# Kernel optimization log

Hardware: AMD Instinct MI355X
Metric: run time of the kernel (lower is better)

The kernel has to match this reference:

```python
import jax, jax.numpy as jnp
import numpy as np

N_NODES = 100000
N_EDGES = 1000000
DIM = 128
N_RELS = 500
N_TIMES = 1000


def setup_inputs() -> dict:
    key = jax.random.key(0)
    ks = jax.random.split(key, 8)
    h = jax.random.normal(ks[0], (N_NODES, DIM), dtype=jnp.float32)
    edge_index = jax.random.randint(ks[1], (2, N_EDGES), 0, N_NODES, dtype=jnp.int64)
    edge_type = jax.random.randint(ks[2], (N_EDGES,), 0, N_RELS, dtype=jnp.int64)
    edge_time = jax.random.randint(ks[3], (N_EDGES,), 0, N_TIMES, dtype=jnp.int64)
    query_rel = 7
    rel_table = jax.random.normal(ks[4], (N_RELS, DIM), dtype=jnp.float32)
    time_table = jax.random.normal(ks[5], (N_TIMES, DIM), dtype=jnp.float32)
    # Linear weights stored as [in, out] so y = x @ W + b
    W1 = jax.random.normal(ks[6], (4 * DIM, DIM), dtype=jnp.float32) * (1.0 / np.sqrt(4 * DIM))
    b1 = jnp.zeros((DIM,), dtype=jnp.float32)
    W2 = jax.random.normal(ks[7], (DIM, 1), dtype=jnp.float32) * (1.0 / np.sqrt(DIM))
    b2 = jnp.zeros((1,), dtype=jnp.float32)
    return {"h": h, "edge_index": edge_index, "edge_type": edge_type,
            "edge_time": edge_time, "query_rel": query_rel,
            "rel_table": rel_table, "time_table": time_table,
            "W1": W1, "b1": b1, "W2": W2, "b2": b2}


def reference(h, edge_index, edge_type, edge_time, query_rel,
              rel_table, time_table, W1, b1, W2, b2):
    src = edge_index[0]                    # [E]
    h_s = h[src]                           # [E, D] gather
    h_r = rel_table[edge_type]             # [E, D] embedding lookup
    h_t = time_table[edge_time]            # [E, D] embedding lookup
    h_rq = jnp.broadcast_to(rel_table[query_rel][None, :], h_s.shape)  # [E, D]
    x = jnp.concatenate([h_s, h_r, h_rq, h_t], axis=1)  # [E, 4D]
    hidden = jax.nn.relu(x @ W1 + b1)      # [E, D]
    alpha = hidden @ W2 + b2               # [E, 1]
    return jax.nn.sigmoid(alpha)[:, 0]     # [E]
```

## Files before the change

kernel.cpp:

```cpp
#include <hip/hip_runtime.h>
#include <hip/hip_fp16.h>
#include <hip/hip_fp8.h>
#include <math.h>

#define DIM 128

typedef _Float16 half8 __attribute__((ext_vector_type(8)));
typedef _Float16 half2v __attribute__((ext_vector_type(2)));
typedef float floatx4 __attribute__((ext_vector_type(4)));


__global__ __launch_bounds__(256) void precompute(
    const float* __restrict__ h, const float* __restrict__ rel,
    const float* __restrict__ tim, const int* __restrict__ qrel,
    const float* __restrict__ W1, const float* __restrict__ b1,
    unsigned char* __restrict__ H8, __half* __restrict__ Rh, __half* __restrict__ Th,
    int n_nodes, int n_rels, int n_times, int nHB, int nRB)
{
    const int tid = threadIdx.x;
    const int b = blockIdx.x;

    const float* A; int M, k0, row0; bool isR = false, isH = false;
    __half* Out = nullptr;
    if (b < nHB)            { A = h;   isH = true; M = n_nodes; k0 = 0;   row0 = b * 128; }
    else if (b < nHB + nRB) { A = rel; Out = Rh;   M = n_rels;  k0 = 128; row0 = (b - nHB) * 128; isR = true; }
    else                    { A = tim; Out = Th;   M = n_times; k0 = 384; row0 = (b - nHB - nRB) * 128; }

    __shared__ _Float16 fragB[32 * 64 * 8];
    __shared__ float c0f[DIM];

#pragma unroll
    for (int it = 0; it < 8; ++it) {
        const int o = tid + it * 256;
        const int ctkc = o >> 6, L = o & 63;
        const int ct = ctkc >> 2, kc = ctkc & 3;
        const int q = L >> 4, n15 = L & 15;
        const float* base = W1 + (size_t)(k0 + kc * 32 + q * 8) * DIM + ct * 16 + n15;
        half8 f;
#pragma unroll
        for (int j = 0; j < 8; ++j) f[j] = (_Float16)base[(size_t)j * DIM];
        *(half8*)&fragB[o * 8] = f;
    }
    if (isR && tid < DIM) {
        const int q = qrel[0];
        const float* hq = rel + (size_t)q * DIM;
        float s = b1[tid];
        for (int k = 0; k < DIM; ++k)
            s = fmaf(hq[k], W1[(size_t)(256 + k) * DIM + tid], s);
        c0f[tid] = s;
    }
    __syncthreads();

    const int w = tid >> 6;
    const int lane = tid & 63;
    const int m15 = lane & 15, q = lane >> 4;

    const float* aBase[2];
#pragma unroll
    for (int mt = 0; mt < 2; ++mt) {
        int arow = row0 + w * 32 + mt * 16 + m15;
        if (arow >= M) arow = M - 1;
        aBase[mt] = A + (size_t)arow * DIM + q * 8;
    }

    floatx4 acc[2][8];
#pragma unroll
    for (int mt = 0; mt < 2; ++mt)
#pragma unroll
        for (int ct = 0; ct < 8; ++ct) acc[mt][ct] = (floatx4)0.f;

#pragma unroll
    for (int kc = 0; kc < 4; ++kc) {
        half8 af[2];
#pragma unroll
        for (int mt = 0; mt < 2; ++mt) {
            const float4 a0 = *(const float4*)(aBase[mt] + kc * 32);
            const float4 a1 = *(const float4*)(aBase[mt] + kc * 32 + 4);
            af[mt][0] = (_Float16)a0.x; af[mt][1] = (_Float16)a0.y;
            af[mt][2] = (_Float16)a0.z; af[mt][3] = (_Float16)a0.w;
            af[mt][4] = (_Float16)a1.x; af[mt][5] = (_Float16)a1.y;
            af[mt][6] = (_Float16)a1.z; af[mt][7] = (_Float16)a1.w;
        }
#pragma unroll
        for (int ct = 0; ct < 8; ++ct) {
            const half8 bf = *(half8*)&fragB[(((ct * 4 + kc) * 64) + lane) * 8];
            acc[0][ct] = __builtin_amdgcn_mfma_f32_16x16x32_f16(af[0], bf, acc[0][ct], 0, 0, 0);
            acc[1][ct] = __builtin_amdgcn_mfma_f32_16x16x32_f16(af[1], bf, acc[1][ct], 0, 0, 0);
        }
    }

    float cadd[8];
#pragma unroll
    for (int ct = 0; ct < 8; ++ct) cadd[ct] = isR ? c0f[ct * 16 + m15] : 0.f;

#pragma unroll
    for (int mt = 0; mt < 2; ++mt)
#pragma unroll
        for (int r = 0; r < 4; ++r) {
            const int m = row0 + w * 32 + mt * 16 + q * 4 + r;
            if (m < M) {
                if (isH) {
                    uint2 pk;
#if __has_builtin(__builtin_amdgcn_cvt_pk_fp8_f32)
                    int w0 = 0, w1 = 0;
                    w0 = __builtin_amdgcn_cvt_pk_fp8_f32(acc[mt][0][r], acc[mt][1][r], w0, false);
                    w0 = __builtin_amdgcn_cvt_pk_fp8_f32(acc[mt][2][r], acc[mt][3][r], w0, true);
                    w1 = __builtin_amdgcn_cvt_pk_fp8_f32(acc[mt][4][r], acc[mt][5][r], w1, false);
                    w1 = __builtin_amdgcn_cvt_pk_fp8_f32(acc[mt][6][r], acc[mt][7][r], w1, true);
                    pk.x = (unsigned)w0; pk.y = (unsigned)w1;
#else
                    union { uint2 u; unsigned char bb[8]; } pu;
#pragma unroll
                    for (int ct = 0; ct < 8; ++ct)
                        pu.bb[ct] = __hip_fp8_e4m3(acc[mt][ct][r]).__x;
                    pk = pu.u;
#endif
                    *(uint2*)(H8 + (size_t)m * DIM + m15 * 8) = pk;
                } else {
                    half8 hv;
#pragma unroll
                    for (int ct = 0; ct < 8; ++ct)
                        hv[ct] = (_Float16)(acc[mt][ct][r] + cadd[ct]);
                    *(half8*)(Out + (size_t)m * DIM + m15 * 8) = hv;
                }
            }
        }
}

__device__ __forceinline__ half2v fp8x2_to_h2(unsigned u16) {
#if __has_builtin(__builtin_amdgcn_cvt_pk_f16_fp8)
    auto c = __builtin_amdgcn_cvt_pk_f16_fp8((short)u16);
    half2v r; r[0] = c[0]; r[1] = c[1];
    return r;
#else
    auto f = __builtin_amdgcn_cvt_pk_f32_fp8((int)u16, false);
    half2v r; r[0] = (_Float16)f[0]; r[1] = (_Float16)f[1];
    return r;
#endif
}

__device__ __forceinline__ float edot(uint2 hu, uint4 ru, uint4 tu,
                                      const half2v* __restrict__ w2h) {
    union U { uint4 u; half2v h[4]; };
    U R, T; R.u = ru; T.u = tu;
    const half2v z = (half2v)(_Float16)0.f;
    const unsigned hw[4] = {hu.x & 0xffffu, hu.x >> 16, hu.y & 0xffffu, hu.y >> 16};
    float p = 0.f;
#pragma unroll
    for (int j = 0; j < 4; ++j) {
        const half2v hh = fp8x2_to_h2(hw[j]);
        half2v s = hh + R.h[j] + T.h[j];
        s = __builtin_elementwise_max(s, z);
#if __has_builtin(__builtin_amdgcn_fdot2)
        p = __builtin_amdgcn_fdot2(s, w2h[j], p, false);
#else
        p = fmaf((float)s[0], (float)w2h[j][0], p);
        p = fmaf((float)s[1], (float)w2h[j][1], p);
#endif
    }
    return p;
}

template<int CTRL>
__device__ __forceinline__ float dpp_row_add(float x) {
    int s = __builtin_amdgcn_update_dpp(0, __float_as_int(x), CTRL, 0xf, 0xf, true);
    return x + __int_as_float(s);
}

__global__ __launch_bounds__(256) void edge_kernel(
    const int* __restrict__ ei, const int* __restrict__ ety,
    const int* __restrict__ eti,
    const unsigned char* __restrict__ H8, const __half* __restrict__ Rh,
    const __half* __restrict__ Th,
    const float* __restrict__ W2, const float* __restrict__ b2,
    float* __restrict__ out, int E, int nGrpTotal)
{
    const int tid = threadIdx.x;
    const int l = tid & 15;
    int g = blockIdx.x * 16 + (tid >> 4);
    const int nQuad = (E + 3) >> 2;
    if (g >= nQuad) return;

    half2v w2h[4];
#pragma unroll
    for (int j = 0; j < 4; ++j) {
        w2h[j][0] = (_Float16)W2[(2 * j) * 16 + l];
        w2h[j][1] = (_Float16)W2[(2 * j + 1) * 16 + l];
    }
    const float b2v = b2[0];
    const bool exact = (E & 3) == 0;
    const unsigned char* Rh8 = (const unsigned char*)Rh;
    const unsigned char* Th8 = (const unsigned char*)Th;

    int s[4], r[4], t[4];
    {
        const int e0 = 4 * g;
        if (exact || e0 + 3 < E) {
#pragma unroll
            for (int i = 0; i < 4; ++i) { s[i] = ei[e0 + i]; r[i] = ety[e0 + i]; t[i] = eti[e0 + i]; }
        } else {
#pragma unroll
            for (int i = 0; i < 4; ++i) {
                const int e = min(e0 + i, E - 1);
                s[i] = ei[e]; r[i] = ety[e]; t[i] = eti[e];
            }
        }
    }

    while (true) {
        const int gn = g + nGrpTotal;
        uint2 hv[4]; uint4 rv[4], tv[4];
#pragma unroll
        for (int i = 0; i < 4; ++i) {
            hv[i] = *(const uint2*)(H8  + ((unsigned)s[i] << 7) + (l << 3));
            rv[i] = *(const uint4*)(Rh8 + ((unsigned)r[i] << 8) + (l << 4));
            tv[i] = *(const uint4*)(Th8 + ((unsigned)t[i] << 8) + (l << 4));
        }
        if (gn < nQuad) {
            const int e0 = 4 * gn;
            if (exact || e0 + 3 < E) {
#pragma unroll
                for (int i = 0; i < 4; ++i) { s[i] = ei[e0 + i]; r[i] = ety[e0 + i]; t[i] = eti[e0 + i]; }
            } else {
#pragma unroll
                for (int i = 0; i < 4; ++i) {
                    const int e = min(e0 + i, E - 1);
                    s[i] = ei[e]; r[i] = ety[e]; t[i] = eti[e];
                }
            }
        }
        float p[4];
#pragma unroll
        for (int i = 0; i < 4; ++i)
            p[i] = edot(hv[i], rv[i], tv[i], w2h);
#pragma unroll
        for (int i = 0; i < 4; ++i) {
            p[i] = dpp_row_add<0x111>(p[i]);
            p[i] = dpp_row_add<0x112>(p[i]);
            p[i] = dpp_row_add<0x114>(p[i]);
            p[i] = dpp_row_add<0x118>(p[i]);
        }
        if (l == 15) {
            const int e0 = 4 * g;
            float4 o;
            o.x = 1.f / (1.f + __expf(-(p[0] + b2v)));
            o.y = 1.f / (1.f + __expf(-(p[1] + b2v)));
            o.z = 1.f / (1.f + __expf(-(p[2] + b2v)));
            o.w = 1.f / (1.f + __expf(-(p[3] + b2v)));
            if (e0 + 3 < E) {
                *(float4*)(out + e0) = o;
            } else {
                const float ov[4] = {o.x, o.y, o.z, o.w};
                for (int i = 0; i < 4 && e0 + i < E; ++i) out[e0 + i] = ov[i];
            }
        }
        if (gn >= nQuad) break;
        g = gn;
    }
}

extern "C" void kernel_launch(void* const* d_in, const int* in_sizes, int n_in,
                              void* d_out, int out_size, void* d_ws, size_t ws_size,
                              hipStream_t stream) {
    const float* h          = (const float*)d_in[0];
    const int*   edge_index = (const int*)d_in[1];
    const int*   edge_type  = (const int*)d_in[2];
    const int*   edge_time  = (const int*)d_in[3];
    const int*   query_rel  = (const int*)d_in[4];
    const float* rel_table  = (const float*)d_in[5];
    const float* time_table = (const float*)d_in[6];
    const float* W1         = (const float*)d_in[7];
    const float* b1         = (const float*)d_in[8];
    const float* W2         = (const float*)d_in[9];
    const float* b2         = (const float*)d_in[10];
    float* out = (float*)d_out;

    const int n_nodes = in_sizes[0] / DIM;
    const int E       = in_sizes[2];
    const int n_rels  = in_sizes[5] / DIM;
    const int n_times = in_sizes[6] / DIM;

    unsigned char* H8 = (unsigned char*)d_ws;
    __half* Rh = (__half*)(H8 + (((size_t)n_nodes * DIM + 255) & ~(size_t)255));
    __half* Th = Rh + (size_t)n_rels * DIM;

    const int nHB = (n_nodes + 127) / 128;
    const int nRB = (n_rels + 127) / 128;
    const int nTB = (n_times + 127) / 128;

    precompute<<<nHB + nRB + nTB, 256, 0, stream>>>(
        h, rel_table, time_table, query_rel, W1, b1,
        H8, Rh, Th, n_nodes, n_rels, n_times, nHB, nRB);

    const int nBlk = 4096;
    edge_kernel<<<nBlk, 256, 0, stream>>>(
        edge_index, edge_type, edge_time, H8, Rh, Th, W2, b2,
        out, E, nBlk * 16);
}
```

Baseline: 160.0 us.

## Cache relation table in LDS and use persistent 1024-thread blocks

The edge kernel now stages the fp16 relation table (500 rows) in shared memory, so relation gathers read LDS instead of global memory. The launch changes to 256 persistent blocks of 1024 threads. Index loads become vectorized nontemporal loads and the output store becomes nontemporal. In exchange each block pays a 128KB LDS fill, and the large LDS footprint limits occupancy to one block per CU.

```diff
diff --git a/kernel.cpp b/kernel.cpp
--- a/kernel.cpp
+++ b/kernel.cpp
@@ -4,10 +4,12 @@
 #include <math.h>
 
 #define DIM 128
+#define LDS_RELS 500
 
 typedef _Float16 half8 __attribute__((ext_vector_type(8)));
 typedef _Float16 half2v __attribute__((ext_vector_type(2)));
 typedef float floatx4 __attribute__((ext_vector_type(4)));
+typedef int intx4 __attribute__((ext_vector_type(4)));
 
 
 __global__ __launch_bounds__(256) void precompute(
@@ -167,95 +169,109 @@
     return x + __int_as_float(s);
 }
 
-__global__ __launch_bounds__(256) void edge_kernel(
+__device__ __forceinline__ void load_idx4(
+    const int* __restrict__ ei, const int* __restrict__ ety,
+    const int* __restrict__ eti, int g, int E, bool exact,
+    int (&s)[4], int (&r)[4], int (&t)[4])
+{
+    const int e0 = 4 * g;
+    if (exact || e0 + 3 < E) {
+        const intx4 a = __builtin_nontemporal_load((const intx4*)(ei + e0));
+        const intx4 b = __builtin_nontemporal_load((const intx4*)(ety + e0));
+        const intx4 c = __builtin_nontemporal_load((const intx4*)(eti + e0));
+#pragma unroll
+        for (int i = 0; i < 4; ++i) { s[i] = a[i]; r[i] = b[i]; t[i] = c[i]; }
+    } else {
+#pragma unroll
+        for (int i = 0; i < 4; ++i) {
+            const int e = min(e0 + i, E - 1);
+            s[i] = ei[e]; r[i] = ety[e]; t[i] = eti[e];
+        }
+    }
+}
+
+__global__ __launch_bounds__(1024) void edge_kernel(
     const int* __restrict__ ei, const int* __restrict__ ety,
     const int* __restrict__ eti,
     const unsigned char* __restrict__ H8, const __half* __restrict__ Rh,
     const __half* __restrict__ Th,
     const float* __restrict__ W2, const float* __restrict__ b2,
-    float* __restrict__ out, int E, int nGrpTotal)
+    float* __restrict__ out, int E, int n_rels, int nGrpTotal)
 {
+    __shared__ uint4 ldsR[LDS_RELS * 16];
+
     const int tid = threadIdx.x;
+
+    {
+        const uint4* Rg = (const uint4*)Rh;
+        const int n4 = min(n_rels, LDS_RELS) * 16;
+        for (int i = tid; i < n4; i += 1024) ldsR[i] = Rg[i];
+    }
+    __syncthreads();
+
     const int l = tid & 15;
-    int g = blockIdx.x * 16 + (tid >> 4);
+    int g = blockIdx.x * 64 + (tid >> 4);
     const int nQuad = (E + 3) >> 2;
-    if (g >= nQuad) return;
-
-    half2v w2h[4];
-#pragma unroll
-    for (int j = 0; j < 4; ++j) {
-        w2h[j][0] = (_Float16)W2[(2 * j) * 16 + l];
-        w2h[j][1] = (_Float16)W2[(2 * j + 1) * 16 + l];
-    }
-    const float b2v = b2[0];
-    const bool exact = (E & 3) == 0;
-    const unsigned char* Rh8 = (const unsigned char*)Rh;
-    const unsigned char* Th8 = (const unsigned char*)Th;
-
-    int s[4], r[4], t[4];
-    {
-        const int e0 = 4 * g;
-        if (exact || e0 + 3 < E) {
-#pragma unroll
-            for (int i = 0; i < 4; ++i) { s[i] = ei[e0 + i]; r[i] = ety[e0 + i]; t[i] = eti[e0 + i]; }
-        } else {
+    if (g < nQuad) {
+        half2v w2h[4];
+#pragma unroll
+        for (int j = 0; j < 4; ++j) {
+            w2h[j][0] = (_Float16)W2[(2 * j) * 16 + l];
+            w2h[j][1] = (_Float16)W2[(2 * j + 1) * 16 + l];
+        }
+        const float b2v = b2[0];
+        const bool exact = (E & 3) == 0;
+        const unsigned char* Th8 = (const unsigned char*)Th;
+        const unsigned char* Rh8 = (const unsigned char*)Rh;
+
+        int s[4], r[4], t[4];
+        load_idx4(ei, ety, eti, g, E, exact, s, r, t);
+
+        while (true) {
+            const int gn = g + nGrpTotal;
+            uint2 hv[4]; uint4 tv[4];
 #pragma unroll
             for (int i = 0; i < 4; ++i) {
-                const int e = min(e0 + i, E - 1);
-                s[i] = ei[e]; r[i] = ety[e]; t[i] = eti[e];
-            }
-        }
-    }
-
-    while (true) {
-        const int gn = g + nGrpTotal;
-        uint2 hv[4]; uint4 rv[4], tv[4];
-#pragma unroll
-        for (int i = 0; i < 4; ++i) {
-            hv[i] = *(const uint2*)(H8  + ((unsigned)s[i] << 7) + (l << 3));
-            rv[i] = *(const uint4*)(Rh8 + ((unsigned)r[i] << 8) + (l << 4));
-            tv[i] = *(const uint4*)(Th8 + ((unsigned)t[i] << 8) + (l << 4));
-        }
-        if (gn < nQuad) {
-            const int e0 = 4 * gn;
-            if (exact || e0 + 3 < E) {
-#pragma unroll
-                for (int i = 0; i < 4; ++i) { s[i] = ei[e0 + i]; r[i] = ety[e0 + i]; t[i] = eti[e0 + i]; }
-            } else {
-#pragma unroll
-                for (int i = 0; i < 4; ++i) {
-                    const int e = min(e0 + i, E - 1);
-                    s[i] = ei[e]; r[i] = ety[e]; t[i] = eti[e];
+                hv[i] = *(const uint2*)(H8  + ((unsigned)s[i] << 7) + (l << 3));
+                tv[i] = *(const uint4*)(Th8 + ((unsigned)t[i] << 8) + (l << 4));
+            }
+            uint4 rv[4];
+#pragma unroll
+            for (int i = 0; i < 4; ++i) {
+                if (r[i] < LDS_RELS) rv[i] = ldsR[(unsigned)r[i] * 16 + l];
+                else rv[i] = *(const uint4*)(Rh8 + ((unsigned)r[i] << 8) + (l << 4));
+            }
+            if (gn < nQuad)
+                load_idx4(ei, ety, eti, gn, E, exact, s, r, t);
+
+            float p[4];
+#pragma unroll
+            for (int i = 0; i < 4; ++i)
+                p[i] = edot(hv[i], rv[i], tv[i], w2h);
+#pragma unroll
+            for (int i = 0; i < 4; ++i) {
+                p[i] = dpp_row_add<0x111>(p[i]);
+                p[i] = dpp_row_add<0x112>(p[i]);
+                p[i] = dpp_row_add<0x114>(p[i]);
+                p[i] = dpp_row_add<0x118>(p[i]);
+            }
+            if (l == 15) {
+                const int e0 = 4 * g;
+                floatx4 o;
+                o[0] = 1.f / (1.f + __expf(-(p[0] + b2v)));
+                o[1] = 1.f / (1.f + __expf(-(p[1] + b2v)));
+                o[2] = 1.f / (1.f + __expf(-(p[2] + b2v)));
+                o[3] = 1.f / (1.f + __expf(-(p[3] + b2v)));
+                if (e0 + 3 < E) {
+                    __builtin_nontemporal_store(o, (floatx4*)(out + e0));
+                } else {
+                    const float ov[4] = {o[0], o[1], o[2], o[3]};
+                    for (int i = 0; i < 4 && e0 + i < E; ++i) out[e0 + i] = ov[i];
                 }
             }
-        }
-        float p[4];
-#pragma unroll
-        for (int i = 0; i < 4; ++i)
-            p[i] = edot(hv[i], rv[i], tv[i], w2h);
-#pragma unroll
-        for (int i = 0; i < 4; ++i) {
-            p[i] = dpp_row_add<0x111>(p[i]);
-            p[i] = dpp_row_add<0x112>(p[i]);
-            p[i] = dpp_row_add<0x114>(p[i]);
-            p[i] = dpp_row_add<0x118>(p[i]);
-        }
-        if (l == 15) {
-            const int e0 = 4 * g;
-            float4 o;
-            o.x = 1.f / (1.f + __expf(-(p[0] + b2v)));
-            o.y = 1.f / (1.f + __expf(-(p[1] + b2v)));
-            o.z = 1.f / (1.f + __expf(-(p[2] + b2v)));
-            o.w = 1.f / (1.f + __expf(-(p[3] + b2v)));
-            if (e0 + 3 < E) {
-                *(float4*)(out + e0) = o;
-            } else {
-                const float ov[4] = {o.x, o.y, o.z, o.w};
-                for (int i = 0; i < 4 && e0 + i < E; ++i) out[e0 + i] = ov[i];
-            }
-        }
-        if (gn >= nQuad) break;
-        g = gn;
+            if (gn >= nQuad) break;
+            g = gn;
+        }
     }
 }
 
@@ -292,8 +308,8 @@
         h, rel_table, time_table, query_rel, W1, b1,
         H8, Rh, Th, n_nodes, n_rels, n_times, nHB, nRB);
 
-    const int nBlk = 4096;
-    edge_kernel<<<nBlk, 256, 0, stream>>>(
+    const int nBlk = 256;
+    edge_kernel<<<nBlk, 1024, 0, stream>>>(
         edge_index, edge_type, edge_time, H8, Rh, Th, W2, b2,
-        out, E, nBlk * 16);
-}
+        out, E, n_rels, nBlk * 64);
+}
```

Result: slower. 163.3 us (+2.0%).

## Bucket edges by source-node range before gather to improve cache locality

Applied to the files above, without the earlier changes.

Adds a histogram, scan and scatter pass that groups edges into up to 8 buckets by source-node index, writing packed (src,type,time,edge id) records. The edge kernel then walks the buckets in order, so gathers from the fp8 node table hit a smaller working set at a time, and it scatters results back by edge id. This costs three extra launches, an extra 16-byte-per-edge write and read, and uncoalesced output stores. A fallback path keeps the original direct kernel when the workspace is too small.

```diff
diff --git a/kernel.cpp b/kernel.cpp
--- a/kernel.cpp
+++ b/kernel.cpp
@@ -4,10 +4,12 @@
 #include <math.h>
 
 #define DIM 128
+#define NBMAX 8
 
 typedef _Float16 half8 __attribute__((ext_vector_type(8)));
 typedef _Float16 half2v __attribute__((ext_vector_type(2)));
 typedef float floatx4 __attribute__((ext_vector_type(4)));
+typedef int intx4 __attribute__((ext_vector_type(4)));
 
 
 __global__ __launch_bounds__(256) void precompute(
@@ -15,10 +17,13 @@
     const float* __restrict__ tim, const int* __restrict__ qrel,
     const float* __restrict__ W1, const float* __restrict__ b1,
     unsigned char* __restrict__ H8, __half* __restrict__ Rh, __half* __restrict__ Th,
-    int n_nodes, int n_rels, int n_times, int nHB, int nRB)
+    int n_nodes, int n_rels, int n_times, int nHB, int nRB,
+    int* __restrict__ hist)
 {
     const int tid = threadIdx.x;
     const int b = blockIdx.x;
+
+    if (hist && b == 0 && tid < NBMAX) hist[tid] = 0;
 
     const float* A; int M, k0, row0; bool isR = false, isH = false;
     __half* Out = nullptr;
@@ -127,6 +132,59 @@
         }
 }
 
+__global__ __launch_bounds__(256) void hist_kernel(
+    const int* __restrict__ ei, int E, int shift, int* __restrict__ hist)
+{
+    __shared__ int lh[NBMAX];
+    if (threadIdx.x < NBMAX) lh[threadIdx.x] = 0;
+    __syncthreads();
+    for (int e = blockIdx.x * 256 + threadIdx.x; e < E; e += gridDim.x * 256)
+        atomicAdd(&lh[(unsigned)ei[e] >> shift], 1);
+    __syncthreads();
+    if (threadIdx.x < NBMAX) atomicAdd(&hist[threadIdx.x], lh[threadIdx.x]);
+}
+
+__global__ void scan_kernel(const int* __restrict__ hist, int* __restrict__ base,
+                            int* __restrict__ cursor, int NB)
+{
+    if (threadIdx.x == 0 && blockIdx.x == 0) {
+        int acc = 0;
+        for (int i = 0; i < NB; ++i) { base[i] = acc; cursor[i] = acc; acc += hist[i]; }
+        base[NB] = acc;
+    }
+}
+
+#define SC_CH 4096
+__global__ __launch_bounds__(256) void scatter_kernel(
+    const int* __restrict__ ei, const int* __restrict__ ety,
+    const int* __restrict__ eti, int E, int shift,
+    int* __restrict__ cursor, intx4* __restrict__ perm)
+{
+    __shared__ int lh[NBMAX], lbase[NBMAX], lpos[NBMAX];
+    const int nBatch = (E + SC_CH - 1) / SC_CH;
+    for (int batch = blockIdx.x; batch < nBatch; batch += gridDim.x) {
+        const int e0 = batch * SC_CH, e1 = min(e0 + SC_CH, E);
+        if (threadIdx.x < NBMAX) lh[threadIdx.x] = 0;
+        __syncthreads();
+        for (int e = e0 + threadIdx.x; e < e1; e += 256)
+            atomicAdd(&lh[(unsigned)ei[e] >> shift], 1);
+        __syncthreads();
+        if (threadIdx.x < NBMAX) {
+            lbase[threadIdx.x] = atomicAdd(&cursor[threadIdx.x], lh[threadIdx.x]);
+            lpos[threadIdx.x] = 0;
+        }
+        __syncthreads();
+        for (int e = e0 + threadIdx.x; e < e1; e += 256) {
+            const int s = ei[e];
+            const int bk = (unsigned)s >> shift;
+            const int p = lbase[bk] + atomicAdd(&lpos[bk], 1);
+            intx4 rec; rec[0] = s; rec[1] = ety[e]; rec[2] = eti[e]; rec[3] = e;
+            __builtin_nontemporal_store(rec, &perm[p]);
+        }
+        __syncthreads();
+    }
+}
+
 __device__ __forceinline__ half2v fp8x2_to_h2(unsigned u16) {
 #if __has_builtin(__builtin_amdgcn_cvt_pk_f16_fp8)
     auto c = __builtin_amdgcn_cvt_pk_f16_fp8((short)u16);
@@ -167,7 +225,69 @@
     return x + __int_as_float(s);
 }
 
-__global__ __launch_bounds__(256) void edge_kernel(
+__global__ __launch_bounds__(256) void edge_kernel_b(
+    const intx4* __restrict__ perm, const int* __restrict__ base, int NB,
+    const unsigned char* __restrict__ H8, const __half* __restrict__ Rh,
+    const __half* __restrict__ Th,
+    const float* __restrict__ W2, const float* __restrict__ b2,
+    float* __restrict__ out, int nGrpTotal)
+{
+    const int tid = threadIdx.x;
+    const int l = tid & 15;
+    const int grp = blockIdx.x * 16 + (tid >> 4);
+
+    half2v w2h[4];
+#pragma unroll
+    for (int j = 0; j < 4; ++j) {
+        w2h[j][0] = (_Float16)W2[(2 * j) * 16 + l];
+        w2h[j][1] = (_Float16)W2[(2 * j + 1) * 16 + l];
+    }
+    const float b2v = b2[0];
+    const unsigned char* Rh8 = (const unsigned char*)Rh;
+    const unsigned char* Th8 = (const unsigned char*)Th;
+
+    for (int k = 0; k < NB; ++k) {
+        const int lo = base[k], hi = base[k + 1];
+        const int nq = (hi - lo + 3) >> 2;
+        for (int qd = grp; qd < nq; qd += nGrpTotal) {
+            const int e0 = lo + 4 * qd;
+            intx4 rec[4];
+#pragma unroll
+            for (int i = 0; i < 4; ++i)
+                rec[i] = __builtin_nontemporal_load(&perm[min(e0 + i, hi - 1)]);
+
+            uint2 hv[4]; uint4 rv[4], tv[4];
+#pragma unroll
+            for (int i = 0; i < 4; ++i) {
+                hv[i] = *(const uint2*)(H8  + ((unsigned)rec[i][0] << 7) + (l << 3));
+                rv[i] = *(const uint4*)(Rh8 + ((unsigned)rec[i][1] << 8) + (l << 4));
+                tv[i] = *(const uint4*)(Th8 + ((unsigned)rec[i][2] << 8) + (l << 4));
+            }
+            float p[4];
+#pragma unroll
+            for (int i = 0; i < 4; ++i)
+                p[i] = edot(hv[i], rv[i], tv[i], w2h);
+#pragma unroll
+            for (int i = 0; i < 4; ++i) {
+                p[i] = dpp_row_add<0x111>(p[i]);
+                p[i] = dpp_row_add<0x112>(p[i]);
+                p[i] = dpp_row_add<0x114>(p[i]);
+                p[i] = dpp_row_add<0x118>(p[i]);
+            }
+            if (l == 15) {
+#pragma unroll
+                for (int i = 0; i < 4; ++i) {
+                    if (e0 + i < hi) {
+                        const float o = 1.f / (1.f + __expf(-(p[i] + b2v)));
+                        __builtin_nontemporal_store(o, out + rec[i][3]);
+                    }
+                }
+            }
+        }
+    }
+}
+
+__global__ __launch_bounds__(256) void edge_kernel_direct(
     const int* __restrict__ ei, const int* __restrict__ ety,
     const int* __restrict__ eti,
     const unsigned char* __restrict__ H8, const __half* __restrict__ Rh,
@@ -242,15 +362,15 @@
         }
         if (l == 15) {
             const int e0 = 4 * g;
-            float4 o;
-            o.x = 1.f / (1.f + __expf(-(p[0] + b2v)));
-            o.y = 1.f / (1.f + __expf(-(p[1] + b2v)));
-            o.z = 1.f / (1.f + __expf(-(p[2] + b2v)));
-            o.w = 1.f / (1.f + __expf(-(p[3] + b2v)));
+            floatx4 o;
+            o[0] = 1.f / (1.f + __expf(-(p[0] + b2v)));
+            o[1] = 1.f / (1.f + __expf(-(p[1] + b2v)));
+            o[2] = 1.f / (1.f + __expf(-(p[2] + b2v)));
+            o[3] = 1.f / (1.f + __expf(-(p[3] + b2v)));
             if (e0 + 3 < E) {
-                *(float4*)(out + e0) = o;
+                *(floatx4*)(out + e0) = o;
             } else {
-                const float ov[4] = {o.x, o.y, o.z, o.w};
+                const float ov[4] = {o[0], o[1], o[2], o[3]};
                 for (int i = 0; i < 4 && e0 + i < E; ++i) out[e0 + i] = ov[i];
             }
         }
@@ -280,9 +400,24 @@
     const int n_rels  = in_sizes[5] / DIM;
     const int n_times = in_sizes[6] / DIM;
 
+    const size_t szH = ((size_t)n_nodes * DIM + 255) & ~(size_t)255;
+    const size_t szR = ((size_t)n_rels * DIM * 2 + 255) & ~(size_t)255;
+    const size_t szT = ((size_t)n_times * DIM * 2 + 255) & ~(size_t)255;
+    const size_t szP = (((size_t)E * 16) + 255) & ~(size_t)255;
     unsigned char* H8 = (unsigned char*)d_ws;
-    __half* Rh = (__half*)(H8 + (((size_t)n_nodes * DIM + 255) & ~(size_t)255));
-    __half* Th = Rh + (size_t)n_rels * DIM;
+    __half* Rh = (__half*)(H8 + szH);
+    __half* Th = (__half*)(H8 + szH + szR);
+    intx4* perm = (intx4*)(H8 + szH + szR + szT);
+    int* counters = (int*)(H8 + szH + szR + szT + szP);
+    const bool bucketed = (szH + szR + szT + szP + 256) <= ws_size;
+
+    int* histP   = counters + 0;
+    int* cursorP = counters + 8;
+    int* baseP   = counters + 16;
+
+    int shift = 0;
+    while (((unsigned)(n_nodes - 1) >> shift) >= NBMAX) ++shift;
+    const int NB = (int)(((unsigned)(n_nodes - 1) >> shift) + 1);
 
     const int nHB = (n_nodes + 127) / 128;
     const int nRB = (n_rels + 127) / 128;
@@ -290,10 +425,22 @@
 
     precompute<<<nHB + nRB + nTB, 256, 0, stream>>>(
         h, rel_table, time_table, query_rel, W1, b1,
-        H8, Rh, Th, n_nodes, n_rels, n_times, nHB, nRB);
-
-    const int nBlk = 4096;
-    edge_kernel<<<nBlk, 256, 0, stream>>>(
-        edge_index, edge_type, edge_time, H8, Rh, Th, W2, b2,
-        out, E, nBlk * 16);
-}
+        H8, Rh, Th, n_nodes, n_rels, n_times, nHB, nRB,
+        bucketed ? histP : nullptr);
+
+    if (bucketed) {
+        hist_kernel<<<256, 256, 0, stream>>>(edge_index, E, shift, histP);
+        scan_kernel<<<1, 64, 0, stream>>>(histP, baseP, cursorP, NB);
+        scatter_kernel<<<256, 256, 0, stream>>>(
+            edge_index, edge_type, edge_time, E, shift, cursorP, perm);
+
+        const int nBlk = 2048;
+        edge_kernel_b<<<nBlk, 256, 0, stream>>>(
+            perm, baseP, NB, H8, Rh, Th, W2, b2, out, nBlk * 16);
+    } else {
+        const int nBlk = 4096;
+        edge_kernel_direct<<<nBlk, 256, 0, stream>>>(
+            edge_index, edge_type, edge_time, H8, Rh, Th, W2, b2,
+            out, E, nBlk * 16);
+    }
+}
```

New measurement: 216.3 us. +35.2%, slower.
